# Kernel tuning notes

Hardware: AMD Instinct MI355X
Metric: run time of the kernel (lower is better)

## Reference

```python
import jax, jax.numpy as jnp
import numpy as np

LN_EPS = 1e-5

def _layernorm(x, g, b):
    mu = jnp.mean(x, axis=-1, keepdims=True)
    var = jnp.var(x, axis=-1, keepdims=True)
    return (x - mu) * jax.lax.rsqrt(var + LN_EPS) * g + b

def setup_inputs() -> dict:
    key = jax.random.key(0)
    ks = jax.random.split(key, 5)
    N, M, A, B = 30000, 12, 256, 128
    atom_feats = jax.random.normal(ks[0], (N, A), dtype=jnp.float32)
    bond_feats = jax.random.normal(ks[1], (N, M, B), dtype=jnp.float32)
    fc_w = jax.random.normal(ks[2], (2 * A, 2 * A + B), dtype=jnp.float32) * 0.02
    fc_b = jax.random.normal(ks[3], (2 * A,), dtype=jnp.float32) * 0.02
    ln1_g = jnp.ones((2 * A,), dtype=jnp.float32)
    ln1_b = jnp.zeros((2 * A,), dtype=jnp.float32)
    ln2_g = jnp.ones((A,), dtype=jnp.float32)
    ln2_b = jnp.zeros((A,), dtype=jnp.float32)
    nbr_indices = jax.random.randint(ks[4], (N, M), 0, N, dtype=jnp.int64)
    return {"atom_feats": atom_feats, "bond_feats": bond_feats, "fc_w": fc_w,
            "fc_b": fc_b, "ln1_g": ln1_g, "ln1_b": ln1_b, "ln2_g": ln2_g,
            "ln2_b": ln2_b, "nbr_indices": nbr_indices}

def reference(atom_feats, bond_feats, fc_w, fc_b, ln1_g, ln1_b, ln2_g, ln2_b, nbr_indices):
    N, M = nbr_indices.shape
    A = atom_feats.shape[-1]
    nbr_feats = atom_feats[nbr_indices]                        # [N, M, A] gather
    atom_expand = jnp.broadcast_to(atom_feats[:, None, :], (N, M, A))
    combined = jnp.concatenate([atom_expand, nbr_feats, bond_feats], axis=-1)  # [N, M, 2A+B]
    z = jnp.einsum('nmd,kd->nmk', combined, fc_w) + fc_b       # [N, M, 2A]
    z = _layernorm(z, ln1_g, ln1_b)
    gate = jax.nn.sigmoid(z[..., :A])
    core = jax.nn.softplus(z[..., A:])
    out = jnp.mean(gate * core, axis=1)                        # [N, A]
    out = _layernorm(out, ln2_g, ln2_b)
    return atom_feats + out
```

## Files before the change

### kernel.cpp

```cpp
#include <hip/hip_runtime.h>
#include <hip/hip_bf16.h>

#define N_ATOMS 30000
#define M_NBR   12
#define A_DIM   256
#define B_DIM   128

typedef __bf16 bf16x8 __attribute__((ext_vector_type(8)));
typedef float  f32x4  __attribute__((ext_vector_type(4)));

__device__ __forceinline__ unsigned pkbf(float a, float b) {
    union { __bf16 h[2]; unsigned u; } r;
    r.h[0] = (__bf16)a; r.h[1] = (__bf16)b;
    return r.u;
}
__device__ __forceinline__ unsigned short f2bf(float f) {
    union { __bf16 h; unsigned short s; } r; r.h = (__bf16)f; return r.s;
}
__device__ __forceinline__ float bflo(unsigned u) { union { unsigned x; float f; } v; v.x = u << 16;          return v.f; }
__device__ __forceinline__ float bfhi(unsigned u) { union { unsigned x; float f; } v; v.x = u & 0xffff0000u;  return v.f; }

__device__ __forceinline__ float fexp2(float x) { return __builtin_amdgcn_exp2f(x); }
__device__ __forceinline__ float flog2(float x) { return __builtin_amdgcn_logf(x); }

__device__ __forceinline__ float rowsum16(float x) {
    union { float f; int i; } a, b;
    a.f = x;
    b.i = __builtin_amdgcn_update_dpp(0, a.i, 0x121, 0xF, 0xF, true); a.f += b.f;
    b.i = __builtin_amdgcn_update_dpp(0, a.i, 0x122, 0xF, 0xF, true); a.f += b.f;
    b.i = __builtin_amdgcn_update_dpp(0, a.i, 0x124, 0xF, 0xF, true); a.f += b.f;
    b.i = __builtin_amdgcn_update_dpp(0, a.i, 0x128, 0xF, 0xF, true); a.f += b.f;
    return a.f;
}

__device__ __forceinline__ int packAddr8(int c) {
    int cc = c & 255;
    int slot = ((cc >> 4) & 1) + ((c >> 8) << 1);
    return (cc >> 5) * 64 + (cc & 15) * 4 + slot;
}

__global__ void pack_weights(const float* __restrict__ fc_w,
                             unsigned short* __restrict__ Wp1,
                             unsigned short* __restrict__ Wp3) {
    int idx = blockIdx.x * 256 + threadIdx.x;
    const int n1 = 32 * 1024 * 8;
    if (idx < n1) {
        int j = idx & 7, n = (idx >> 3) & 1023, g = idx >> 13;
        float v = (n < 512) ? fc_w[n * 640 + g * 8 + j]
                            : fc_w[(n - 512) * 640 + 256 + g * 8 + j];
        Wp1[idx] = f2bf(v);
    } else {
        int k = idx - n1;
        if (k < 16 * 512 * 8) {
            int j = k & 7, n = (k >> 3) & 511, g = k >> 12;
            Wp3[k] = f2bf(fc_w[n * 640 + 512 + g * 8 + j]);
        }
    }
}

__global__ __launch_bounds__(512, 2) void gemm_p(
    const float* __restrict__ atom, const float* __restrict__ fc_b,
    const unsigned short* __restrict__ Wp1, unsigned short* __restrict__ P)
{
    __shared__ unsigned short sA[128 * 256];
    const int tid = threadIdx.x;
    const int r0 = blockIdx.x * 128;
    const int cb = blockIdx.y;

    #pragma unroll
    for (int s = 0; s < 8; ++s) {
        int G = tid + s * 512;
        int row = G >> 5, gc = G & 31;
        int grow = r0 + row;
        uint4 pk;
        if (grow < N_ATOMS) {
            const float4* src = reinterpret_cast<const float4*>(atom + (size_t)grow * 256 + gc * 8);
            float4 v0 = src[0], v1 = src[1];
            pk.x = pkbf(v0.x, v0.y); pk.y = pkbf(v0.z, v0.w);
            pk.z = pkbf(v1.x, v1.y); pk.w = pkbf(v1.z, v1.w);
        } else {
            pk = make_uint4(0u, 0u, 0u, 0u);
        }
        *reinterpret_cast<uint4*>(&sA[row * 256 + ((gc ^ (row & 7)) << 3)]) = pk;
    }
    __syncthreads();

    const int lane = tid & 63, wave = tid >> 6;
    const int wr = wave >> 2, wcc = wave & 3;
    const int l15 = lane & 15, l16 = lane >> 4;

    f32x4 acc[4][8];
    #pragma unroll
    for (int mt = 0; mt < 4; ++mt)
        #pragma unroll
        for (int nt = 0; nt < 8; ++nt) acc[mt][nt] = f32x4{0.f, 0.f, 0.f, 0.f};

    #pragma unroll
    for (int ks = 0; ks < 8; ++ks) {
        bf16x8 af[4];
        #pragma unroll
        for (int mt = 0; mt < 4; ++mt) {
            int row = wr * 64 + mt * 16 + l15;
            int g = ks * 4 + l16;
            af[mt] = *reinterpret_cast<const bf16x8*>(&sA[row * 256 + ((g ^ (row & 7)) << 3)]);
        }
        bf16x8 bfr[8];
        #pragma unroll
        for (int nt = 0; nt < 8; ++nt) {
            int col = cb * 512 + wcc * 128 + nt * 16 + l15;
            bfr[nt] = *reinterpret_cast<const bf16x8*>(&Wp1[((size_t)(ks * 4 + l16) * 1024 + col) * 8]);
        }
        #pragma unroll
        for (int mt = 0; mt < 4; ++mt)
            #pragma unroll
            for (int nt = 0; nt < 8; ++nt)
                acc[mt][nt] = __builtin_amdgcn_mfma_f32_16x16x32_bf16(af[mt], bfr[nt], acc[mt][nt], 0, 0, 0);
    }

    #pragma unroll
    for (int np = 0; np < 4; ++np) {
        int zc0 = wcc * 128 + np * 32 + l15;
        float b0 = (cb == 0) ? fc_b[zc0] : 0.f;
        float b1 = (cb == 0) ? fc_b[zc0 + 16] : 0.f;
        int pa = cb * 512 + packAddr8(zc0);
        #pragma unroll
        for (int mt = 0; mt < 4; ++mt) {
            #pragma unroll
            for (int j = 0; j < 4; ++j) {
                int row = r0 + wr * 64 + mt * 16 + l16 * 4 + j;
                if (row < N_ATOMS)
                    *reinterpret_cast<unsigned*>(&P[(size_t)row * 1024 + pa]) =
                        pkbf(acc[mt][2 * np][j] + b0, acc[mt][2 * np + 1][j] + b1);
            }
        }
    }
}

__global__ __launch_bounds__(512, 4) void fused_conv(
    const float* __restrict__ atom, const float* __restrict__ bond,
    const int* __restrict__ nbr, const unsigned short* __restrict__ P,
    const unsigned short* __restrict__ Wp3,
    const float* __restrict__ ln1_g, const float* __restrict__ ln1_b,
    const float* __restrict__ ln2_g, const float* __restrict__ ln2_b,
    float* __restrict__ out)
{
    __shared__ unsigned short sA[48 * 128];
    __shared__ float sRed[2][48][9];
    __shared__ float2 sStat[48];
    __shared__ float sO[4][256];

    const int tid = threadIdx.x;
    const int i0 = blockIdx.x * 4;
    const int lane = tid & 63, wc = tid >> 6;
    const int l15 = lane & 15, l16 = lane >> 4;
    const float L2E = 1.4426950408889634f;

    { float* so = &sO[0][0]; so[tid] = 0.f; so[tid + 512] = 0.f; }

    int4 nbq0 = *reinterpret_cast<const int4*>(&nbr[i0 * 12 +      l16 * 4]);
    int4 nbq1 = *reinterpret_cast<const int4*>(&nbr[i0 * 12 + 16 + l16 * 4]);
    int4 nbq2 = *reinterpret_cast<const int4*>(&nbr[i0 * 12 + 32 + l16 * 4]);

    float4 bv[2][2];
    #pragma unroll
    for (int s = 0; s < 2; ++s) {
        int G = tid + s * 512;
        if (G < 768) {
            int row = G >> 4, gc = G & 15;
            const float4* src = reinterpret_cast<const float4*>(bond + (size_t)(i0 * 12 + row) * 128 + gc * 8);
            bv[s][0] = src[0]; bv[s][1] = src[1];
        }
    }

    const char* Pb = reinterpret_cast<const char*>(P);
    const unsigned cOff = (unsigned)(wc * 128 + l15 * 8);
    uint2 p2q[12];
    {
        const int* n0 = reinterpret_cast<const int*>(&nbq0);
        const int* n1 = reinterpret_cast<const int*>(&nbq1);
        const int* n2 = reinterpret_cast<const int*>(&nbq2);
        #pragma unroll
        for (int j = 0; j < 4; ++j) {
            p2q[j]     = *reinterpret_cast<const uint2*>(Pb + ((unsigned)n0[j] * 2048u + 1024u + cOff));
            p2q[4 + j] = *reinterpret_cast<const uint2*>(Pb + ((unsigned)n1[j] * 2048u + 1024u + cOff));
            p2q[8 + j] = *reinterpret_cast<const uint2*>(Pb + ((unsigned)n2[j] * 2048u + 1024u + cOff));
        }
    }
    uint2 p1q[3];
    #pragma unroll
    for (int mt = 0; mt < 3; ++mt) {
        unsigned li = (unsigned)((mt * 16 + l16 * 4) / 12);
        p1q[mt] = *reinterpret_cast<const uint2*>(Pb + (((unsigned)i0 + li) * 2048u + cOff));
    }

    #pragma unroll
    for (int s = 0; s < 2; ++s) {
        int G = tid + s * 512;
        if (G < 768) {
            int row = G >> 4, gc = G & 15;
            uint4 pk;
            pk.x = pkbf(bv[s][0].x, bv[s][0].y); pk.y = pkbf(bv[s][0].z, bv[s][0].w);
            pk.z = pkbf(bv[s][1].x, bv[s][1].y); pk.w = pkbf(bv[s][1].z, bv[s][1].w);
            *reinterpret_cast<uint4*>(&sA[row * 128 + ((gc ^ (row & 7)) << 3)]) = pk;
        }
    }

    f32x4 acc[3][4];
    #pragma unroll
    for (int mt = 0; mt < 3; ++mt) {
        uint2 c1 = p1q[mt];
        float p1v[4] = { bflo(c1.x), bfhi(c1.x), bflo(c1.y), bfhi(c1.y) };
        #pragma unroll
        for (int j = 0; j < 4; ++j) {
            uint2 c2 = p2q[mt * 4 + j];
            acc[mt][0][j] = p1v[0] + bflo(c2.x);
            acc[mt][1][j] = p1v[1] + bfhi(c2.x);
            acc[mt][2][j] = p1v[2] + bflo(c2.y);
            acc[mt][3][j] = p1v[3] + bfhi(c2.y);
        }
    }
    __syncthreads();

    #pragma unroll
    for (int ks = 0; ks < 4; ++ks) {
        bf16x8 af[3];
        #pragma unroll
        for (int mt = 0; mt < 3; ++mt) {
            int row = mt * 16 + l15;
            int g = ks * 4 + l16;
            af[mt] = *reinterpret_cast<const bf16x8*>(&sA[row * 128 + ((g ^ (row & 7)) << 3)]);
        }
        bf16x8 bfr[4];
        #pragma unroll
        for (int nt = 0; nt < 4; ++nt) {
            int col = (nt < 2) ? (wc * 32 + nt * 16 + l15)
                               : (256 + wc * 32 + (nt - 2) * 16 + l15);
            bfr[nt] = *reinterpret_cast<const bf16x8*>(&Wp3[((size_t)(ks * 4 + l16) * 512 + col) * 8]);
        }
        #pragma unroll
        for (int mt = 0; mt < 3; ++mt)
            #pragma unroll
            for (int nt = 0; nt < 4; ++nt)
                acc[mt][nt] = __builtin_amdgcn_mfma_f32_16x16x32_bf16(af[mt], bfr[nt], acc[mt][nt], 0, 0, 0);
    }

    #pragma unroll
    for (int mt = 0; mt < 3; ++mt) {
        #pragma unroll
        for (int j = 0; j < 4; ++j) {
            const int row = mt * 16 + l16 * 4 + j;
            float z0 = acc[mt][0][j], z1 = acc[mt][1][j];
            float z2 = acc[mt][2][j], z3 = acc[mt][3][j];
            float s = (z0 + z1) + (z2 + z3);
            float q = fmaf(z0, z0, fmaf(z1, z1, fmaf(z2, z2, z3 * z3)));
            s = rowsum16(s);
            q = rowsum16(q);
            if (l15 == 0) { sRed[0][row][wc] = s; sRed[1][row][wc] = q; }
        }
    }

    float g1[2], gC[2], l2b1[2], l2bC[2];
    #pragma unroll
    for (int nt = 0; nt < 2; ++nt) {
        int a = wc * 32 + nt * 16 + l15;
        g1[nt] = ln1_g[a];       l2b1[nt] = ln1_b[a] * L2E;
        gC[nt] = ln1_g[256 + a]; l2bC[nt] = ln1_b[256 + a] * L2E;
    }
    __syncthreads();

    if (tid < 48) {
        float s4 = 0.f, q4 = 0.f;
        #pragma unroll
        for (int w = 0; w < 8; ++w) { s4 += sRed[0][tid][w]; q4 += sRed[1][tid][w]; }
        float mu = s4 * (1.f / 512.f);
        float var = q4 * (1.f / 512.f) - mu * mu;
        float rs = __builtin_amdgcn_rsqf(var + 1e-5f) * L2E;
        sStat[tid] = make_float2(rs, mu * rs);
    }
    __syncthreads();

    #pragma unroll
    for (int mt = 0; mt < 3; ++mt) {
        const int li = (mt * 16 + l16 * 4) / 12;
        float2 st[4];
        #pragma unroll
        for (int j = 0; j < 4; ++j) st[j] = sStat[mt * 16 + l16 * 4 + j];
        #pragma unroll
        for (int nt = 0; nt < 2; ++nt) {
            float tq = 0.f;
            #pragma unroll
            for (int j = 0; j < 4; ++j) {
                float ug = fmaf(fmaf(acc[mt][nt][j],     st[j].x, -st[j].y), g1[nt], l2b1[nt]);
                float uc = fmaf(fmaf(acc[mt][nt + 2][j], st[j].x, -st[j].y), gC[nt], l2bC[nt]);
                float gt  = __builtin_amdgcn_rcpf(1.f + fexp2(-ug));
                float sp2 = flog2(1.f + fexp2(uc));
                tq = fmaf(gt, sp2, tq);
            }
            atomicAdd(&sO[li][wc * 32 + nt * 16 + l15], tq);
        }
    }
    __syncthreads();

    if (wc < 4) {
        const int gi = i0 + wc;
        float v[4]; float s = 0.f, q = 0.f;
        #pragma unroll
        for (int qd = 0; qd < 4; ++qd) {
            v[qd] = sO[wc][lane + qd * 64];
            s += v[qd]; q = fmaf(v[qd], v[qd], q);
        }
        #pragma unroll
        for (int msk = 1; msk <= 32; msk <<= 1) {
            s += __shfl_xor(s, msk, 64);
            q += __shfl_xor(q, msk, 64);
        }
        float mu = s * (1.f / 256.f);
        float var = q * (1.f / 256.f) - mu * mu;
        float rstd = __builtin_amdgcn_rsqf(var + 1e-5f);
        #pragma unroll
        for (int qd = 0; qd < 4; ++qd) {
            int a = lane + qd * 64;
            out[(size_t)gi * 256 + a] = atom[(size_t)gi * 256 + a]
                                      + (v[qd] - mu) * rstd * ln2_g[a] + ln2_b[a];
        }
    }
}

extern "C" void kernel_launch(void* const* d_in, const int* in_sizes, int n_in,
                              void* d_out, int out_size, void* d_ws, size_t ws_size,
                              hipStream_t stream) {
    const float* atom  = (const float*)d_in[0];
    const float* bond  = (const float*)d_in[1];
    const float* fc_w  = (const float*)d_in[2];
    const float* fc_b  = (const float*)d_in[3];
    const float* ln1_g = (const float*)d_in[4];
    const float* ln1_b = (const float*)d_in[5];
    const float* ln2_g = (const float*)d_in[6];
    const float* ln2_b = (const float*)d_in[7];
    const int*   nbr   = (const int*)d_in[8];

    char* ws = (char*)d_ws;
    unsigned short* P   = (unsigned short*)ws;
    unsigned short* Wp1 = (unsigned short*)(ws + 61440000);
    unsigned short* Wp3 = (unsigned short*)(ws + 61440000 + 524288);
    float* outp = (float*)d_out;

    hipLaunchKernelGGL(pack_weights, dim3(1280), dim3(256), 0, stream, fc_w, Wp1, Wp3);
    hipLaunchKernelGGL(gemm_p, dim3(235, 2), dim3(512), 0, stream, atom, fc_b, Wp1, P);
    hipLaunchKernelGGL(fused_conv, dim3(7500), dim3(512), 0, stream,
                       atom, bond, nbr, P, Wp3, ln1_g, ln1_b, ln2_g, ln2_b, outp);
}
```

Baseline: 273.0 us.

## Gather neighbor projections into LDS via async global_load_lds, add after MFMA

Rather than each lane gathering 8-byte fragments of the projected neighbor and self rows into registers, each wave issues full-row 16-byte-per-lane global_load_lds transfers into a new padded LDS buffer. The MFMA accumulation now starts from zero, and the gathered P values are read from LDS and added after the matrix multiply, so the gather latency can overlap the bond GEMM. The MFMA loop is also reordered to load B fragments in pairs, which lowers register pressure. The cost is about 54KB of extra shared memory per block, which may limit occupancy below the requested 4 blocks per CU.

```diff
diff --git a/kernel.cpp b/kernel.cpp
--- a/kernel.cpp
+++ b/kernel.cpp
@@ -8,6 +8,10 @@
 
 typedef __bf16 bf16x8 __attribute__((ext_vector_type(8)));
 typedef float  f32x4  __attribute__((ext_vector_type(4)));
+
+#define GLOAD_LDS16(g, l) __builtin_amdgcn_global_load_lds( \
+    (const __attribute__((address_space(1))) unsigned int*)(const void*)(g), \
+    (__attribute__((address_space(3))) unsigned int*)(void*)(l), 16, 0, 0)
 
 __device__ __forceinline__ unsigned pkbf(float a, float b) {
     union { __bf16 h[2]; unsigned u; } r;
@@ -136,6 +140,7 @@
     }
 }
 
+#define SP_STRIDE 1040
 __global__ __launch_bounds__(512, 4) void fused_conv(
     const float* __restrict__ atom, const float* __restrict__ bond,
     const int* __restrict__ nbr, const unsigned short* __restrict__ P,
@@ -145,6 +150,7 @@
     float* __restrict__ out)
 {
     __shared__ unsigned short sA[48 * 128];
+    __shared__ __align__(16) unsigned char sP[52 * SP_STRIDE];
     __shared__ float sRed[2][48][9];
     __shared__ float2 sStat[48];
     __shared__ float sO[4][256];
@@ -154,12 +160,21 @@
     const int lane = tid & 63, wc = tid >> 6;
     const int l15 = lane & 15, l16 = lane >> 4;
     const float L2E = 1.4426950408889634f;
+    const char* Pb = reinterpret_cast<const char*>(P);
 
     { float* so = &sO[0][0]; so[tid] = 0.f; so[tid + 512] = 0.f; }
 
-    int4 nbq0 = *reinterpret_cast<const int4*>(&nbr[i0 * 12 +      l16 * 4]);
-    int4 nbq1 = *reinterpret_cast<const int4*>(&nbr[i0 * 12 + 16 + l16 * 4]);
-    int4 nbq2 = *reinterpret_cast<const int4*>(&nbr[i0 * 12 + 32 + l16 * 4]);
+    {
+        const unsigned lane16 = (unsigned)lane * 16u;
+        #pragma unroll
+        for (int k = 0; k < 6; ++k) {
+            int r = wc + k * 8;
+            int nb = nbr[i0 * 12 + r];
+            GLOAD_LDS16(Pb + (unsigned)nb * 2048u + 1024u + lane16, &sP[r * SP_STRIDE]);
+        }
+        if (wc < 4)
+            GLOAD_LDS16(Pb + (unsigned)(i0 + wc) * 2048u + lane16, &sP[(48 + wc) * SP_STRIDE]);
+    }
 
     float4 bv[2][2];
     #pragma unroll
@@ -171,28 +186,6 @@
             bv[s][0] = src[0]; bv[s][1] = src[1];
         }
     }
-
-    const char* Pb = reinterpret_cast<const char*>(P);
-    const unsigned cOff = (unsigned)(wc * 128 + l15 * 8);
-    uint2 p2q[12];
-    {
-        const int* n0 = reinterpret_cast<const int*>(&nbq0);
-        const int* n1 = reinterpret_cast<const int*>(&nbq1);
-        const int* n2 = reinterpret_cast<const int*>(&nbq2);
-        #pragma unroll
-        for (int j = 0; j < 4; ++j) {
-            p2q[j]     = *reinterpret_cast<const uint2*>(Pb + ((unsigned)n0[j] * 2048u + 1024u + cOff));
-            p2q[4 + j] = *reinterpret_cast<const uint2*>(Pb + ((unsigned)n1[j] * 2048u + 1024u + cOff));
-            p2q[8 + j] = *reinterpret_cast<const uint2*>(Pb + ((unsigned)n2[j] * 2048u + 1024u + cOff));
-        }
-    }
-    uint2 p1q[3];
-    #pragma unroll
-    for (int mt = 0; mt < 3; ++mt) {
-        unsigned li = (unsigned)((mt * 16 + l16 * 4) / 12);
-        p1q[mt] = *reinterpret_cast<const uint2*>(Pb + (((unsigned)i0 + li) * 2048u + cOff));
-    }
-
     #pragma unroll
     for (int s = 0; s < 2; ++s) {
         int G = tid + s * 512;
@@ -204,53 +197,49 @@
             *reinterpret_cast<uint4*>(&sA[row * 128 + ((gc ^ (row & 7)) << 3)]) = pk;
         }
     }
+    __syncthreads();
 
     f32x4 acc[3][4];
     #pragma unroll
+    for (int mt = 0; mt < 3; ++mt)
+        #pragma unroll
+        for (int nt = 0; nt < 4; ++nt) acc[mt][nt] = f32x4{0.f, 0.f, 0.f, 0.f};
+
+    #pragma unroll
+    for (int ks = 0; ks < 4; ++ks) {
+        #pragma unroll
+        for (int p = 0; p < 2; ++p) {
+            bf16x8 b0 = *reinterpret_cast<const bf16x8*>(
+                &Wp3[((size_t)(ks * 4 + l16) * 512 + p * 256 + wc * 32 + l15) * 8]);
+            bf16x8 b1 = *reinterpret_cast<const bf16x8*>(
+                &Wp3[((size_t)(ks * 4 + l16) * 512 + p * 256 + wc * 32 + 16 + l15) * 8]);
+            #pragma unroll
+            for (int mt = 0; mt < 3; ++mt) {
+                int row = mt * 16 + l15;
+                bf16x8 af = *reinterpret_cast<const bf16x8*>(
+                    &sA[row * 128 + (((ks * 4 + l16) ^ (row & 7)) << 3)]);
+                acc[mt][2 * p]     = __builtin_amdgcn_mfma_f32_16x16x32_bf16(af, b0, acc[mt][2 * p], 0, 0, 0);
+                acc[mt][2 * p + 1] = __builtin_amdgcn_mfma_f32_16x16x32_bf16(af, b1, acc[mt][2 * p + 1], 0, 0, 0);
+            }
+        }
+    }
+
+    const unsigned cOff = (unsigned)(wc * 128 + l15 * 8);
+    #pragma unroll
     for (int mt = 0; mt < 3; ++mt) {
-        uint2 c1 = p1q[mt];
+        const int liRow = 48 + (mt * 16 + l16 * 4) / 12;
+        uint2 c1 = *reinterpret_cast<const uint2*>(&sP[liRow * SP_STRIDE + cOff]);
         float p1v[4] = { bflo(c1.x), bfhi(c1.x), bflo(c1.y), bfhi(c1.y) };
-        #pragma unroll
-        for (int j = 0; j < 4; ++j) {
-            uint2 c2 = p2q[mt * 4 + j];
-            acc[mt][0][j] = p1v[0] + bflo(c2.x);
-            acc[mt][1][j] = p1v[1] + bfhi(c2.x);
-            acc[mt][2][j] = p1v[2] + bflo(c2.y);
-            acc[mt][3][j] = p1v[3] + bfhi(c2.y);
-        }
-    }
-    __syncthreads();
-
-    #pragma unroll
-    for (int ks = 0; ks < 4; ++ks) {
-        bf16x8 af[3];
-        #pragma unroll
-        for (int mt = 0; mt < 3; ++mt) {
-            int row = mt * 16 + l15;
-            int g = ks * 4 + l16;
-            af[mt] = *reinterpret_cast<const bf16x8*>(&sA[row * 128 + ((g ^ (row & 7)) << 3)]);
-        }
-        bf16x8 bfr[4];
-        #pragma unroll
-        for (int nt = 0; nt < 4; ++nt) {
-            int col = (nt < 2) ? (wc * 32 + nt * 16 + l15)
-                               : (256 + wc * 32 + (nt - 2) * 16 + l15);
-            bfr[nt] = *reinterpret_cast<const bf16x8*>(&Wp3[((size_t)(ks * 4 + l16) * 512 + col) * 8]);
-        }
-        #pragma unroll
-        for (int mt = 0; mt < 3; ++mt)
-            #pragma unroll
-            for (int nt = 0; nt < 4; ++nt)
-                acc[mt][nt] = __builtin_amdgcn_mfma_f32_16x16x32_bf16(af[mt], bfr[nt], acc[mt][nt], 0, 0, 0);
-    }
-
-    #pragma unroll
-    for (int mt = 0; mt < 3; ++mt) {
         #pragma unroll
         for (int j = 0; j < 4; ++j) {
             const int row = mt * 16 + l16 * 4 + j;
-            float z0 = acc[mt][0][j], z1 = acc[mt][1][j];
-            float z2 = acc[mt][2][j], z3 = acc[mt][3][j];
+            uint2 c2 = *reinterpret_cast<const uint2*>(&sP[row * SP_STRIDE + cOff]);
+            float z0 = acc[mt][0][j] + p1v[0] + bflo(c2.x);
+            float z1 = acc[mt][1][j] + p1v[1] + bfhi(c2.x);
+            float z2 = acc[mt][2][j] + p1v[2] + bflo(c2.y);
+            float z3 = acc[mt][3][j] + p1v[3] + bfhi(c2.y);
+            acc[mt][0][j] = z0; acc[mt][1][j] = z1;
+            acc[mt][2][j] = z2; acc[mt][3][j] = z3;
             float s = (z0 + z1) + (z2 + z3);
             float q = fmaf(z0, z0, fmaf(z1, z1, fmaf(z2, z2, z3 * z3)));
             s = rowsum16(s);
```

Measured after the change: 281.7 us. +3.2%, slower.

## Process two atom groups per block with prefetch of the second group's loads

Applied to the files above, without the earlier changes.

The fused conv kernel now handles 8 atoms per block in two sequential 4-atom phases. The second phase's gathers from P and its bond loads are issued right after the first phase's MFMA tile, so their latency overlaps the first phase's LayerNorm and activation work. Shared buffers for sA and sO are doubled and the grid is halved. Bond loading changes to one float4 per thread over three slots, and the MFMA loop is reordered to load fewer B fragments at once. The cost is more register pressure from the prefetched data and fewer blocks to spread across the GPU.

```diff
diff --git a/kernel.cpp b/kernel.cpp
--- a/kernel.cpp
+++ b/kernel.cpp
@@ -3,8 +3,6 @@
 
 #define N_ATOMS 30000
 #define M_NBR   12
-#define A_DIM   256
-#define B_DIM   128
 
 typedef __bf16 bf16x8 __attribute__((ext_vector_type(8)));
 typedef float  f32x4  __attribute__((ext_vector_type(4)));
@@ -136,76 +134,46 @@
     }
 }
 
-__global__ __launch_bounds__(512, 4) void fused_conv(
-    const float* __restrict__ atom, const float* __restrict__ bond,
-    const int* __restrict__ nbr, const unsigned short* __restrict__ P,
-    const unsigned short* __restrict__ Wp3,
-    const float* __restrict__ ln1_g, const float* __restrict__ ln1_b,
-    const float* __restrict__ ln2_g, const float* __restrict__ ln2_b,
-    float* __restrict__ out)
-{
-    __shared__ unsigned short sA[48 * 128];
-    __shared__ float sRed[2][48][9];
-    __shared__ float2 sStat[48];
-    __shared__ float sO[4][256];
-
-    const int tid = threadIdx.x;
-    const int i0 = blockIdx.x * 4;
-    const int lane = tid & 63, wc = tid >> 6;
-    const int l15 = lane & 15, l16 = lane >> 4;
-    const float L2E = 1.4426950408889634f;
-
-    { float* so = &sO[0][0]; so[tid] = 0.f; so[tid + 512] = 0.f; }
-
+__device__ __forceinline__ void bondLoad(const float* __restrict__ bond, int i0, int tid, float4 bv[3]) {
+    #pragma unroll
+    for (int s = 0; s < 3; ++s) {
+        int g = tid + s * 512;
+        int row = g >> 5, gc = g & 31;
+        bv[s] = *reinterpret_cast<const float4*>(bond + (size_t)(i0 * 12 + row) * 128 + gc * 4);
+    }
+}
+__device__ __forceinline__ void bondWrite(const float4 bv[3], int tid, unsigned short* sAbuf) {
+    #pragma unroll
+    for (int s = 0; s < 3; ++s) {
+        int g = tid + s * 512;
+        int row = g >> 5, gc = g & 31;
+        uint2 pk;
+        pk.x = pkbf(bv[s].x, bv[s].y); pk.y = pkbf(bv[s].z, bv[s].w);
+        int elem = (((gc >> 1) ^ (row & 7)) << 3) + ((gc & 1) << 2);
+        *reinterpret_cast<uint2*>(&sAbuf[row * 128 + elem]) = pk;
+    }
+}
+__device__ __forceinline__ void loadP(const char* __restrict__ Pb, const int* __restrict__ nbr,
+                                      int i0, int l16, unsigned cOff, uint2 p2q[12], uint2 p1q[3]) {
     int4 nbq0 = *reinterpret_cast<const int4*>(&nbr[i0 * 12 +      l16 * 4]);
     int4 nbq1 = *reinterpret_cast<const int4*>(&nbr[i0 * 12 + 16 + l16 * 4]);
     int4 nbq2 = *reinterpret_cast<const int4*>(&nbr[i0 * 12 + 32 + l16 * 4]);
-
-    float4 bv[2][2];
-    #pragma unroll
-    for (int s = 0; s < 2; ++s) {
-        int G = tid + s * 512;
-        if (G < 768) {
-            int row = G >> 4, gc = G & 15;
-            const float4* src = reinterpret_cast<const float4*>(bond + (size_t)(i0 * 12 + row) * 128 + gc * 8);
-            bv[s][0] = src[0]; bv[s][1] = src[1];
-        }
-    }
-
-    const char* Pb = reinterpret_cast<const char*>(P);
-    const unsigned cOff = (unsigned)(wc * 128 + l15 * 8);
-    uint2 p2q[12];
-    {
-        const int* n0 = reinterpret_cast<const int*>(&nbq0);
-        const int* n1 = reinterpret_cast<const int*>(&nbq1);
-        const int* n2 = reinterpret_cast<const int*>(&nbq2);
-        #pragma unroll
-        for (int j = 0; j < 4; ++j) {
-            p2q[j]     = *reinterpret_cast<const uint2*>(Pb + ((unsigned)n0[j] * 2048u + 1024u + cOff));
-            p2q[4 + j] = *reinterpret_cast<const uint2*>(Pb + ((unsigned)n1[j] * 2048u + 1024u + cOff));
-            p2q[8 + j] = *reinterpret_cast<const uint2*>(Pb + ((unsigned)n2[j] * 2048u + 1024u + cOff));
-        }
-    }
-    uint2 p1q[3];
+    const int* n0 = reinterpret_cast<const int*>(&nbq0);
+    const int* n1 = reinterpret_cast<const int*>(&nbq1);
+    const int* n2 = reinterpret_cast<const int*>(&nbq2);
+    #pragma unroll
+    for (int j = 0; j < 4; ++j) {
+        p2q[j]     = *reinterpret_cast<const uint2*>(Pb + ((unsigned)n0[j] * 2048u + 1024u + cOff));
+        p2q[4 + j] = *reinterpret_cast<const uint2*>(Pb + ((unsigned)n1[j] * 2048u + 1024u + cOff));
+        p2q[8 + j] = *reinterpret_cast<const uint2*>(Pb + ((unsigned)n2[j] * 2048u + 1024u + cOff));
+    }
     #pragma unroll
     for (int mt = 0; mt < 3; ++mt) {
         unsigned li = (unsigned)((mt * 16 + l16 * 4) / 12);
         p1q[mt] = *reinterpret_cast<const uint2*>(Pb + (((unsigned)i0 + li) * 2048u + cOff));
     }
-
-    #pragma unroll
-    for (int s = 0; s < 2; ++s) {
-        int G = tid + s * 512;
-        if (G < 768) {
-            int row = G >> 4, gc = G & 15;
-            uint4 pk;
-            pk.x = pkbf(bv[s][0].x, bv[s][0].y); pk.y = pkbf(bv[s][0].z, bv[s][0].w);
-            pk.z = pkbf(bv[s][1].x, bv[s][1].y); pk.w = pkbf(bv[s][1].z, bv[s][1].w);
-            *reinterpret_cast<uint4*>(&sA[row * 128 + ((gc ^ (row & 7)) << 3)]) = pk;
-        }
-    }
-
-    f32x4 acc[3][4];
+}
+__device__ __forceinline__ void accInit(const uint2 p2q[12], const uint2 p1q[3], f32x4 acc[3][4]) {
     #pragma unroll
     for (int mt = 0; mt < 3; ++mt) {
         uint2 c1 = p1q[mt];
@@ -219,31 +187,31 @@
             acc[mt][3][j] = p1v[3] + bfhi(c2.y);
         }
     }
-    __syncthreads();
-
+}
+__device__ __forceinline__ void gemmTile(const unsigned short* __restrict__ sAbuf,
+                                         const unsigned short* __restrict__ Wp3,
+                                         int l15, int l16, int wc, f32x4 acc[3][4]) {
     #pragma unroll
     for (int ks = 0; ks < 4; ++ks) {
-        bf16x8 af[3];
-        #pragma unroll
-        for (int mt = 0; mt < 3; ++mt) {
-            int row = mt * 16 + l15;
-            int g = ks * 4 + l16;
-            af[mt] = *reinterpret_cast<const bf16x8*>(&sA[row * 128 + ((g ^ (row & 7)) << 3)]);
-        }
-        bf16x8 bfr[4];
-        #pragma unroll
-        for (int nt = 0; nt < 4; ++nt) {
-            int col = (nt < 2) ? (wc * 32 + nt * 16 + l15)
-                               : (256 + wc * 32 + (nt - 2) * 16 + l15);
-            bfr[nt] = *reinterpret_cast<const bf16x8*>(&Wp3[((size_t)(ks * 4 + l16) * 512 + col) * 8]);
-        }
-        #pragma unroll
-        for (int mt = 0; mt < 3; ++mt)
+        #pragma unroll
+        for (int p = 0; p < 2; ++p) {
+            bf16x8 b0 = *reinterpret_cast<const bf16x8*>(
+                &Wp3[((size_t)(ks * 4 + l16) * 512 + p * 256 + wc * 32 + l15) * 8]);
+            bf16x8 b1 = *reinterpret_cast<const bf16x8*>(
+                &Wp3[((size_t)(ks * 4 + l16) * 512 + p * 256 + wc * 32 + 16 + l15) * 8]);
             #pragma unroll
-            for (int nt = 0; nt < 4; ++nt)
-                acc[mt][nt] = __builtin_amdgcn_mfma_f32_16x16x32_bf16(af[mt], bfr[nt], acc[mt][nt], 0, 0, 0);
-    }
-
+            for (int mt = 0; mt < 3; ++mt) {
+                int row = mt * 16 + l15;
+                bf16x8 af = *reinterpret_cast<const bf16x8*>(
+                    &sAbuf[row * 128 + (((ks * 4 + l16) ^ (row & 7)) << 3)]);
+                acc[mt][2 * p]     = __builtin_amdgcn_mfma_f32_16x16x32_bf16(af, b0, acc[mt][2 * p], 0, 0, 0);
+                acc[mt][2 * p + 1] = __builtin_amdgcn_mfma_f32_16x16x32_bf16(af, b1, acc[mt][2 * p + 1], 0, 0, 0);
+            }
+        }
+    }
+}
+__device__ __forceinline__ void pass1Stats(const f32x4 acc[3][4], float (*sRed)[48][9],
+                                           int l16, int l15, int wc) {
     #pragma unroll
     for (int mt = 0; mt < 3; ++mt) {
         #pragma unroll
@@ -258,16 +226,8 @@
             if (l15 == 0) { sRed[0][row][wc] = s; sRed[1][row][wc] = q; }
         }
     }
-
-    float g1[2], gC[2], l2b1[2], l2bC[2];
-    #pragma unroll
-    for (int nt = 0; nt < 2; ++nt) {
-        int a = wc * 32 + nt * 16 + l15;
-        g1[nt] = ln1_g[a];       l2b1[nt] = ln1_b[a] * L2E;
-        gC[nt] = ln1_g[256 + a]; l2bC[nt] = ln1_b[256 + a] * L2E;
-    }
-    __syncthreads();
-
+}
+__device__ __forceinline__ void miniReduce(int tid, float (*sRed)[48][9], float2* sStat, float L2E) {
     if (tid < 48) {
         float s4 = 0.f, q4 = 0.f;
         #pragma unroll
@@ -277,8 +237,11 @@
         float rs = __builtin_amdgcn_rsqf(var + 1e-5f) * L2E;
         sStat[tid] = make_float2(rs, mu * rs);
     }
-    __syncthreads();
-
+}
+__device__ __forceinline__ void pass2(const f32x4 acc[3][4], const float2* sStat,
+                                      const float g1[2], const float gC[2],
+                                      const float l2b1[2], const float l2bC[2],
+                                      float (*sObuf)[256], int l16, int l15, int wc) {
     #pragma unroll
     for (int mt = 0; mt < 3; ++mt) {
         const int li = (mt * 16 + l16 * 4) / 12;
@@ -296,17 +259,20 @@
                 float sp2 = flog2(1.f + fexp2(uc));
                 tq = fmaf(gt, sp2, tq);
             }
-            atomicAdd(&sO[li][wc * 32 + nt * 16 + l15], tq);
-        }
-    }
-    __syncthreads();
-
+            atomicAdd(&sObuf[li][wc * 32 + nt * 16 + l15], tq);
+        }
+    }
+}
+__device__ __forceinline__ void ln2Out(const float (*sObuf)[256], int i0, int wc, int lane,
+                                       const float* __restrict__ atom,
+                                       const float* __restrict__ ln2_g, const float* __restrict__ ln2_b,
+                                       float* __restrict__ out) {
     if (wc < 4) {
         const int gi = i0 + wc;
         float v[4]; float s = 0.f, q = 0.f;
         #pragma unroll
         for (int qd = 0; qd < 4; ++qd) {
-            v[qd] = sO[wc][lane + qd * 64];
+            v[qd] = sObuf[wc][lane + qd * 64];
             s += v[qd]; q = fmaf(v[qd], v[qd], q);
         }
         #pragma unroll
@@ -324,6 +290,75 @@
                                       + (v[qd] - mu) * rstd * ln2_g[a] + ln2_b[a];
         }
     }
+}
+
+__global__ __launch_bounds__(512, 4) void fused_conv(
+    const float* __restrict__ atom, const float* __restrict__ bond,
+    const int* __restrict__ nbr, const unsigned short* __restrict__ P,
+    const unsigned short* __restrict__ Wp3,
+    const float* __restrict__ ln1_g, const float* __restrict__ ln1_b,
+    const float* __restrict__ ln2_g, const float* __restrict__ ln2_b,
+    float* __restrict__ out)
+{
+    __shared__ unsigned short sA[2][48 * 128];
+    __shared__ float sRed[2][48][9];
+    __shared__ float2 sStat[48];
+    __shared__ float sO[2][4][256];
+
+    const int tid = threadIdx.x;
+    const int i00 = blockIdx.x * 8;
+    const int i01 = i00 + 4;
+    const int lane = tid & 63, wc = tid >> 6;
+    const int l15 = lane & 15, l16 = lane >> 4;
+    const float L2E = 1.4426950408889634f;
+    const char* Pb = reinterpret_cast<const char*>(P);
+    const unsigned cOff = (unsigned)(wc * 128 + l15 * 8);
+
+    {
+        float* so = &sO[0][0][0];
+        so[tid] = 0.f; so[tid + 512] = 0.f; so[tid + 1024] = 0.f; so[tid + 1536] = 0.f;
+    }
+
+    float4 bv[3];
+    bondLoad(bond, i00, tid, bv);
+    uint2 p2q[12], p1q[3];
+    loadP(Pb, nbr, i00, l16, cOff, p2q, p1q);
+    bondWrite(bv, tid, sA[0]);
+    f32x4 acc[3][4];
+    accInit(p2q, p1q, acc);
+    __syncthreads();
+    gemmTile(sA[0], Wp3, l15, l16, wc, acc);
+
+    uint2 P2b[12], P1b[3];
+    loadP(Pb, nbr, i01, l16, cOff, P2b, P1b);
+    float4 bvb[3];
+    bondLoad(bond, i01, tid, bvb);
+
+    pass1Stats(acc, sRed, l16, l15, wc);
+    bondWrite(bvb, tid, sA[1]);
+    float g1[2], gC[2], l2b1[2], l2bC[2];
+    #pragma unroll
+    for (int nt = 0; nt < 2; ++nt) {
+        int a = wc * 32 + nt * 16 + l15;
+        g1[nt] = ln1_g[a];       l2b1[nt] = ln1_b[a] * L2E;
+        gC[nt] = ln1_g[256 + a]; l2bC[nt] = ln1_b[256 + a] * L2E;
+    }
+    __syncthreads();
+    miniReduce(tid, sRed, sStat, L2E);
+    __syncthreads();
+    pass2(acc, sStat, g1, gC, l2b1, l2bC, sO[0], l16, l15, wc);
+    __syncthreads();
+    ln2Out(sO[0], i00, wc, lane, atom, ln2_g, ln2_b, out);
+
+    accInit(P2b, P1b, acc);
+    gemmTile(sA[1], Wp3, l15, l16, wc, acc);
+    pass1Stats(acc, sRed, l16, l15, wc);
+    __syncthreads();
+    miniReduce(tid, sRed, sStat, L2E);
+    __syncthreads();
+    pass2(acc, sStat, g1, gC, l2b1, l2bC, sO[1], l16, l15, wc);
+    __syncthreads();
+    ln2Out(sO[1], i01, wc, lane, atom, ln2_g, ln2_b, out);
 }
 
 extern "C" void kernel_launch(void* const* d_in, const int* in_sizes, int n_in,
@@ -347,6 +382,6 @@
 
     hipLaunchKernelGGL(pack_weights, dim3(1280), dim3(256), 0, stream, fc_w, Wp1, Wp3);
     hipLaunchKernelGGL(gemm_p, dim3(235, 2), dim3(512), 0, stream, atom, fc_b, Wp1, P);
-    hipLaunchKernelGGL(fused_conv, dim3(7500), dim3(512), 0, stream,
+    hipLaunchKernelGGL(fused_conv, dim3(3750), dim3(512), 0, stream,
                        atom, bond, nbr, P, Wp3, ln1_g, ln1_b, ln2_g, ln2_b, outp);
 }
```

Result: slower. 286.2 us (+4.8%).

## Shrink fused_conv blocks to two atoms with 4 waves and register reductions

Applied to the files above, without the earlier changes.

Restructures fused_conv to process 2 atoms per block with 256 threads (4 waves each covering 64 columns) instead of 4 atoms with 512 threads. The LDS atomics for the neighbor mean are replaced by register accumulation plus cross-lane shuffles. The LN1 stats pass and one __syncthreads are removed by having every lane recompute row statistics from shared partials. This lowers per-block LDS use and synchronization, and each wave now reuses its A fragments over more columns. In exchange the MFMA tile carries 8 padded zero rows (24 real rows in 32) and each thread holds more accumulator registers.

```diff
diff --git a/kernel.cpp b/kernel.cpp
--- a/kernel.cpp
+++ b/kernel.cpp
@@ -3,8 +3,6 @@
 
 #define N_ATOMS 30000
 #define M_NBR   12
-#define A_DIM   256
-#define B_DIM   128
 
 typedef __bf16 bf16x8 __attribute__((ext_vector_type(8)));
 typedef float  f32x4  __attribute__((ext_vector_type(4)));
@@ -136,7 +134,7 @@
     }
 }
 
-__global__ __launch_bounds__(512, 4) void fused_conv(
+__global__ __launch_bounds__(256, 4) void fused_conv(
     const float* __restrict__ atom, const float* __restrict__ bond,
     const int* __restrict__ nbr, const unsigned short* __restrict__ P,
     const unsigned short* __restrict__ Wp3,
@@ -144,185 +142,223 @@
     const float* __restrict__ ln2_g, const float* __restrict__ ln2_b,
     float* __restrict__ out)
 {
-    __shared__ unsigned short sA[48 * 128];
-    __shared__ float sRed[2][48][9];
-    __shared__ float2 sStat[48];
-    __shared__ float sO[4][256];
+    __shared__ unsigned short sA[32 * 128];
+    __shared__ __align__(16) float sRed[2][32][4];
+    __shared__ __align__(16) float sL2[2][2][4];
 
     const int tid = threadIdx.x;
-    const int i0 = blockIdx.x * 4;
+    const int i0 = blockIdx.x * 2;
     const int lane = tid & 63, wc = tid >> 6;
     const int l15 = lane & 15, l16 = lane >> 4;
     const float L2E = 1.4426950408889634f;
-
-    { float* so = &sO[0][0]; so[tid] = 0.f; so[tid + 512] = 0.f; }
-
-    int4 nbq0 = *reinterpret_cast<const int4*>(&nbr[i0 * 12 +      l16 * 4]);
-    int4 nbq1 = *reinterpret_cast<const int4*>(&nbr[i0 * 12 + 16 + l16 * 4]);
-    int4 nbq2 = *reinterpret_cast<const int4*>(&nbr[i0 * 12 + 32 + l16 * 4]);
-
-    float4 bv[2][2];
-    #pragma unroll
-    for (int s = 0; s < 2; ++s) {
-        int G = tid + s * 512;
-        if (G < 768) {
-            int row = G >> 4, gc = G & 15;
-            const float4* src = reinterpret_cast<const float4*>(bond + (size_t)(i0 * 12 + row) * 128 + gc * 8);
-            bv[s][0] = src[0]; bv[s][1] = src[1];
-        }
-    }
-
     const char* Pb = reinterpret_cast<const char*>(P);
-    const unsigned cOff = (unsigned)(wc * 128 + l15 * 8);
-    uint2 p2q[12];
+    const unsigned cOffA = (unsigned)(wc * 256 + l15 * 8);
+    const unsigned cOffB = cOffA + 128u;
+
+    float4 bv[3];
+    #pragma unroll
+    for (int s = 0; s < 3; ++s) {
+        int g = tid + s * 256;
+        int row = g >> 5, gc = g & 31;
+        bv[s] = *reinterpret_cast<const float4*>(bond + (size_t)(i0 * 12 + row) * 128 + gc * 4);
+    }
+
+    int4 nbq0 = *reinterpret_cast<const int4*>(&nbr[i0 * 12 + l16 * 4]);
+    int off16 = (l16 < 2) ? (16 + l16 * 4) : 20;
+    int4 nbq1 = *reinterpret_cast<const int4*>(&nbr[i0 * 12 + off16]);
+
+    uint2 p2q[2][4][2];
     {
         const int* n0 = reinterpret_cast<const int*>(&nbq0);
         const int* n1 = reinterpret_cast<const int*>(&nbq1);
-        const int* n2 = reinterpret_cast<const int*>(&nbq2);
         #pragma unroll
         for (int j = 0; j < 4; ++j) {
-            p2q[j]     = *reinterpret_cast<const uint2*>(Pb + ((unsigned)n0[j] * 2048u + 1024u + cOff));
-            p2q[4 + j] = *reinterpret_cast<const uint2*>(Pb + ((unsigned)n1[j] * 2048u + 1024u + cOff));
-            p2q[8 + j] = *reinterpret_cast<const uint2*>(Pb + ((unsigned)n2[j] * 2048u + 1024u + cOff));
-        }
-    }
-    uint2 p1q[3];
-    #pragma unroll
-    for (int mt = 0; mt < 3; ++mt) {
-        unsigned li = (unsigned)((mt * 16 + l16 * 4) / 12);
-        p1q[mt] = *reinterpret_cast<const uint2*>(Pb + (((unsigned)i0 + li) * 2048u + cOff));
-    }
-
-    #pragma unroll
-    for (int s = 0; s < 2; ++s) {
-        int G = tid + s * 512;
-        if (G < 768) {
-            int row = G >> 4, gc = G & 15;
-            uint4 pk;
-            pk.x = pkbf(bv[s][0].x, bv[s][0].y); pk.y = pkbf(bv[s][0].z, bv[s][0].w);
-            pk.z = pkbf(bv[s][1].x, bv[s][1].y); pk.w = pkbf(bv[s][1].z, bv[s][1].w);
-            *reinterpret_cast<uint4*>(&sA[row * 128 + ((gc ^ (row & 7)) << 3)]) = pk;
-        }
-    }
-
-    f32x4 acc[3][4];
-    #pragma unroll
-    for (int mt = 0; mt < 3; ++mt) {
-        uint2 c1 = p1q[mt];
-        float p1v[4] = { bflo(c1.x), bfhi(c1.x), bflo(c1.y), bfhi(c1.y) };
+            unsigned b0 = (unsigned)n0[j] * 2048u + 1024u;
+            p2q[0][j][0] = *reinterpret_cast<const uint2*>(Pb + b0 + cOffA);
+            p2q[0][j][1] = *reinterpret_cast<const uint2*>(Pb + b0 + cOffB);
+            unsigned b1 = (unsigned)n1[j] * 2048u + 1024u;
+            p2q[1][j][0] = *reinterpret_cast<const uint2*>(Pb + b1 + cOffA);
+            p2q[1][j][1] = *reinterpret_cast<const uint2*>(Pb + b1 + cOffB);
+        }
+    }
+    uint2 p1q[2][2];
+    {
+        unsigned a0 = (unsigned)(i0 + ((l16 < 3) ? 0 : 1)) * 2048u;
+        p1q[0][0] = *reinterpret_cast<const uint2*>(Pb + a0 + cOffA);
+        p1q[0][1] = *reinterpret_cast<const uint2*>(Pb + a0 + cOffB);
+        unsigned a1 = (unsigned)(i0 + 1) * 2048u;
+        p1q[1][0] = *reinterpret_cast<const uint2*>(Pb + a1 + cOffA);
+        p1q[1][1] = *reinterpret_cast<const uint2*>(Pb + a1 + cOffB);
+    }
+
+    #pragma unroll
+    for (int s = 0; s < 3; ++s) {
+        int g = tid + s * 256;
+        int row = g >> 5, gc = g & 31;
+        uint2 pk;
+        pk.x = pkbf(bv[s].x, bv[s].y); pk.y = pkbf(bv[s].z, bv[s].w);
+        int elem = (((gc >> 1) ^ (row & 7)) << 3) + ((gc & 1) << 2);
+        *reinterpret_cast<uint2*>(&sA[row * 128 + elem]) = pk;
+    }
+    {
+        int row = 24 + (tid >> 5), gc = tid & 31;
+        *reinterpret_cast<uint2*>(&sA[row * 128 + gc * 4]) = make_uint2(0u, 0u);
+    }
+
+    f32x4 acc[2][8];
+    #pragma unroll
+    for (int mt = 0; mt < 2; ++mt)
+        #pragma unroll
+        for (int np = 0; np < 2; ++np) {
+            uint2 c1 = p1q[mt][np];
+            float pg0 = bflo(c1.x), pg1 = bfhi(c1.x);
+            float pc0 = bflo(c1.y), pc1 = bfhi(c1.y);
+            #pragma unroll
+            for (int j = 0; j < 4; ++j) {
+                uint2 c2 = p2q[mt][j][np];
+                acc[mt][np * 2 + 0][j]     = pg0 + bflo(c2.x);
+                acc[mt][np * 2 + 1][j]     = pg1 + bfhi(c2.x);
+                acc[mt][4 + np * 2 + 0][j] = pc0 + bflo(c2.y);
+                acc[mt][4 + np * 2 + 1][j] = pc1 + bfhi(c2.y);
+            }
+        }
+    __syncthreads();
+
+    #pragma unroll
+    for (int ks = 0; ks < 4; ++ks) {
+        bf16x8 af[2];
+        #pragma unroll
+        for (int mt = 0; mt < 2; ++mt) {
+            int row = mt * 16 + l15;
+            af[mt] = *reinterpret_cast<const bf16x8*>(
+                &sA[row * 128 + (((ks * 4 + l16) ^ (row & 7)) << 3)]);
+        }
+        #pragma unroll
+        for (int p = 0; p < 2; ++p)
+            #pragma unroll
+            for (int np = 0; np < 2; ++np) {
+                int colbase = p * 256 + wc * 64 + np * 32 + l15;
+                bf16x8 b0 = *reinterpret_cast<const bf16x8*>(
+                    &Wp3[((size_t)(ks * 4 + l16) * 512 + colbase) * 8]);
+                bf16x8 b1 = *reinterpret_cast<const bf16x8*>(
+                    &Wp3[((size_t)(ks * 4 + l16) * 512 + colbase + 16) * 8]);
+                #pragma unroll
+                for (int mt = 0; mt < 2; ++mt) {
+                    acc[mt][p * 4 + np * 2 + 0] = __builtin_amdgcn_mfma_f32_16x16x32_bf16(
+                        af[mt], b0, acc[mt][p * 4 + np * 2 + 0], 0, 0, 0);
+                    acc[mt][p * 4 + np * 2 + 1] = __builtin_amdgcn_mfma_f32_16x16x32_bf16(
+                        af[mt], b1, acc[mt][p * 4 + np * 2 + 1], 0, 0, 0);
+                }
+            }
+    }
+
+    #pragma unroll
+    for (int mt = 0; mt < 2; ++mt)
         #pragma unroll
         for (int j = 0; j < 4; ++j) {
-            uint2 c2 = p2q[mt * 4 + j];
-            acc[mt][0][j] = p1v[0] + bflo(c2.x);
-            acc[mt][1][j] = p1v[1] + bfhi(c2.x);
-            acc[mt][2][j] = p1v[2] + bflo(c2.y);
-            acc[mt][3][j] = p1v[3] + bfhi(c2.y);
-        }
-    }
-    __syncthreads();
-
-    #pragma unroll
-    for (int ks = 0; ks < 4; ++ks) {
-        bf16x8 af[3];
-        #pragma unroll
-        for (int mt = 0; mt < 3; ++mt) {
-            int row = mt * 16 + l15;
-            int g = ks * 4 + l16;
-            af[mt] = *reinterpret_cast<const bf16x8*>(&sA[row * 128 + ((g ^ (row & 7)) << 3)]);
-        }
-        bf16x8 bfr[4];
-        #pragma unroll
-        for (int nt = 0; nt < 4; ++nt) {
-            int col = (nt < 2) ? (wc * 32 + nt * 16 + l15)
-                               : (256 + wc * 32 + (nt - 2) * 16 + l15);
-            bfr[nt] = *reinterpret_cast<const bf16x8*>(&Wp3[((size_t)(ks * 4 + l16) * 512 + col) * 8]);
-        }
-        #pragma unroll
-        for (int mt = 0; mt < 3; ++mt)
-            #pragma unroll
-            for (int nt = 0; nt < 4; ++nt)
-                acc[mt][nt] = __builtin_amdgcn_mfma_f32_16x16x32_bf16(af[mt], bfr[nt], acc[mt][nt], 0, 0, 0);
-    }
-
-    #pragma unroll
-    for (int mt = 0; mt < 3; ++mt) {
-        #pragma unroll
-        for (int j = 0; j < 4; ++j) {
-            const int row = mt * 16 + l16 * 4 + j;
-            float z0 = acc[mt][0][j], z1 = acc[mt][1][j];
-            float z2 = acc[mt][2][j], z3 = acc[mt][3][j];
-            float s = (z0 + z1) + (z2 + z3);
-            float q = fmaf(z0, z0, fmaf(z1, z1, fmaf(z2, z2, z3 * z3)));
+            int row = mt * 16 + l16 * 4 + j;
+            float s = 0.f, q = 0.f;
+            #pragma unroll
+            for (int nt = 0; nt < 8; ++nt) {
+                float z = acc[mt][nt][j];
+                s += z; q = fmaf(z, z, q);
+            }
             s = rowsum16(s);
             q = rowsum16(q);
             if (l15 == 0) { sRed[0][row][wc] = s; sRed[1][row][wc] = q; }
         }
-    }
-
-    float g1[2], gC[2], l2b1[2], l2bC[2];
-    #pragma unroll
-    for (int nt = 0; nt < 2; ++nt) {
-        int a = wc * 32 + nt * 16 + l15;
-        g1[nt] = ln1_g[a];       l2b1[nt] = ln1_b[a] * L2E;
-        gC[nt] = ln1_g[256 + a]; l2bC[nt] = ln1_b[256 + a] * L2E;
-    }
+
+    float g1[4], gC[4], l2b1[4], l2bC[4];
+    #pragma unroll
+    for (int np = 0; np < 2; ++np)
+        #pragma unroll
+        for (int b = 0; b < 2; ++b) {
+            int nt = np * 2 + b;
+            int a = wc * 64 + np * 32 + b * 16 + l15;
+            g1[nt] = ln1_g[a];       l2b1[nt] = ln1_b[a] * L2E;
+            gC[nt] = ln1_g[256 + a]; l2bC[nt] = ln1_b[256 + a] * L2E;
+        }
     __syncthreads();
 
-    if (tid < 48) {
-        float s4 = 0.f, q4 = 0.f;
-        #pragma unroll
-        for (int w = 0; w < 8; ++w) { s4 += sRed[0][tid][w]; q4 += sRed[1][tid][w]; }
-        float mu = s4 * (1.f / 512.f);
-        float var = q4 * (1.f / 512.f) - mu * mu;
-        float rs = __builtin_amdgcn_rsqf(var + 1e-5f) * L2E;
-        sStat[tid] = make_float2(rs, mu * rs);
-    }
-    __syncthreads();
-
-    #pragma unroll
-    for (int mt = 0; mt < 3; ++mt) {
-        const int li = (mt * 16 + l16 * 4) / 12;
-        float2 st[4];
-        #pragma unroll
-        for (int j = 0; j < 4; ++j) st[j] = sStat[mt * 16 + l16 * 4 + j];
-        #pragma unroll
-        for (int nt = 0; nt < 2; ++nt) {
+    float pa0[4] = {0.f, 0.f, 0.f, 0.f};
+    float pa1[4] = {0.f, 0.f, 0.f, 0.f};
+    #pragma unroll
+    for (int mt = 0; mt < 2; ++mt) {
+        float rs[4], mr[4];
+        #pragma unroll
+        for (int j = 0; j < 4; ++j) {
+            int row = mt * 16 + l16 * 4 + j;
+            float4 s4 = *reinterpret_cast<const float4*>(&sRed[0][row][0]);
+            float4 q4 = *reinterpret_cast<const float4*>(&sRed[1][row][0]);
+            float ssum = (s4.x + s4.y) + (s4.z + s4.w);
+            float qsum = (q4.x + q4.y) + (q4.z + q4.w);
+            float mu = ssum * (1.f / 512.f);
+            float var = qsum * (1.f / 512.f) - mu * mu;
+            float r = __builtin_amdgcn_rsqf(var + 1e-5f) * L2E;
+            rs[j] = r; mr[j] = mu * r;
+        }
+        #pragma unroll
+        for (int nt = 0; nt < 4; ++nt) {
             float tq = 0.f;
             #pragma unroll
             for (int j = 0; j < 4; ++j) {
-                float ug = fmaf(fmaf(acc[mt][nt][j],     st[j].x, -st[j].y), g1[nt], l2b1[nt]);
-                float uc = fmaf(fmaf(acc[mt][nt + 2][j], st[j].x, -st[j].y), gC[nt], l2bC[nt]);
+                float ug = fmaf(fmaf(acc[mt][nt][j],     rs[j], -mr[j]), g1[nt], l2b1[nt]);
+                float uc = fmaf(fmaf(acc[mt][nt + 4][j], rs[j], -mr[j]), gC[nt], l2bC[nt]);
                 float gt  = __builtin_amdgcn_rcpf(1.f + fexp2(-ug));
                 float sp2 = flog2(1.f + fexp2(uc));
                 tq = fmaf(gt, sp2, tq);
             }
-            atomicAdd(&sO[li][wc * 32 + nt * 16 + l15], tq);
+            if (mt == 0) {
+                if (l16 < 3) pa0[nt] += tq; else pa1[nt] += tq;
+            } else {
+                if (l16 < 2) pa1[nt] += tq;
+            }
+        }
+    }
+    #pragma unroll
+    for (int nt = 0; nt < 4; ++nt) {
+        pa0[nt] += __shfl_xor(pa0[nt], 16, 64);
+        pa0[nt] += __shfl_xor(pa0[nt], 32, 64);
+        pa1[nt] += __shfl_xor(pa1[nt], 16, 64);
+        pa1[nt] += __shfl_xor(pa1[nt], 32, 64);
+    }
+
+    {
+        float s0 = (pa0[0] + pa0[1]) + (pa0[2] + pa0[3]);
+        float q0 = fmaf(pa0[0], pa0[0], fmaf(pa0[1], pa0[1], fmaf(pa0[2], pa0[2], pa0[3] * pa0[3])));
+        float s1 = (pa1[0] + pa1[1]) + (pa1[2] + pa1[3]);
+        float q1 = fmaf(pa1[0], pa1[0], fmaf(pa1[1], pa1[1], fmaf(pa1[2], pa1[2], pa1[3] * pa1[3])));
+        s0 = rowsum16(s0); q0 = rowsum16(q0);
+        s1 = rowsum16(s1); q1 = rowsum16(q1);
+        if (lane == 0) {
+            sL2[0][0][wc] = s0; sL2[0][1][wc] = q0;
+            sL2[1][0][wc] = s1; sL2[1][1][wc] = q1;
         }
     }
     __syncthreads();
 
-    if (wc < 4) {
-        const int gi = i0 + wc;
-        float v[4]; float s = 0.f, q = 0.f;
-        #pragma unroll
-        for (int qd = 0; qd < 4; ++qd) {
-            v[qd] = sO[wc][lane + qd * 64];
-            s += v[qd]; q = fmaf(v[qd], v[qd], q);
-        }
-        #pragma unroll
-        for (int msk = 1; msk <= 32; msk <<= 1) {
-            s += __shfl_xor(s, msk, 64);
-            q += __shfl_xor(q, msk, 64);
-        }
-        float mu = s * (1.f / 256.f);
-        float var = q * (1.f / 256.f) - mu * mu;
+    if (l16 < 2) {
+        const int a = l16;
+        const int gi = i0 + a;
+        float4 sv = *reinterpret_cast<const float4*>(&sL2[a][0][0]);
+        float4 qv = *reinterpret_cast<const float4*>(&sL2[a][1][0]);
+        float ssum = (sv.x + sv.y) + (sv.z + sv.w);
+        float qsum = (qv.x + qv.y) + (qv.z + qv.w);
+        float mu = ssum * (1.f / 256.f);
+        float var = qsum * (1.f / 256.f) - mu * mu;
         float rstd = __builtin_amdgcn_rsqf(var + 1e-5f);
-        #pragma unroll
-        for (int qd = 0; qd < 4; ++qd) {
-            int a = lane + qd * 64;
-            out[(size_t)gi * 256 + a] = atom[(size_t)gi * 256 + a]
-                                      + (v[qd] - mu) * rstd * ln2_g[a] + ln2_b[a];
-        }
+        float vv[4];
+        #pragma unroll
+        for (int nt = 0; nt < 4; ++nt) vv[nt] = (l16 == 0) ? pa0[nt] : pa1[nt];
+        #pragma unroll
+        for (int np = 0; np < 2; ++np)
+            #pragma unroll
+            for (int b = 0; b < 2; ++b) {
+                int nt = np * 2 + b;
+                int c = wc * 64 + np * 32 + b * 16 + l15;
+                out[(size_t)gi * 256 + c] = atom[(size_t)gi * 256 + c]
+                                          + (vv[nt] - mu) * rstd * ln2_g[c] + ln2_b[c];
+            }
     }
 }
 
@@ -347,6 +383,6 @@
 
     hipLaunchKernelGGL(pack_weights, dim3(1280), dim3(256), 0, stream, fc_w, Wp1, Wp3);
     hipLaunchKernelGGL(gemm_p, dim3(235, 2), dim3(512), 0, stream, atom, fc_b, Wp1, P);
-    hipLaunchKernelGGL(fused_conv, dim3(7500), dim3(512), 0, stream,
+    hipLaunchKernelGGL(fused_conv, dim3(15000), dim3(256), 0, stream,
                        atom, bond, nbr, P, Wp3, ln1_g, ln1_b, ln2_g, ln2_b, outp);
 }
```

Measured after the change: 239.7 us. -12.2%, faster.
